# Performance work log

Measured on AMD Instinct MI355X. Metric: run time of the kernel, lower is better.

Reference implementation:

```python
import jax, jax.numpy as jnp
import numpy as np

NUM_ITER = 20
EPS = 1e-8


def _conv(x, w, pad):
    # x: [N, Cin, H, W], w: [Cout, Cin, kh, kw] (cross-correlation, like torch conv2d)
    return jax.lax.conv_general_dilated(
        x, w, window_strides=(1, 1), padding=pad,
        dimension_numbers=('NCHW', 'OIHW', 'NCHW'))


def setup_inputs() -> dict:
    key = jax.random.key(0)
    x = jax.random.normal(key, (2, 4, 3, 256, 256), dtype=jnp.float32)
    return {
        'x': x,
        'lam': jnp.array([0.02], dtype=jnp.float32),
        'tau': jnp.array([0.25], dtype=jnp.float32),
        'theta': jnp.array([0.1], dtype=jnp.float32),
        'wx': jnp.array([[-1.0, 1.0, 0.0]], dtype=jnp.float32),
        'wy': jnp.array([[-1.0], [1.0], [0.0]], dtype=jnp.float32),
    }


def reference(x, lam, tau, theta, wx, wy):
    # x: [2, B, C, H, W] -> pairs of single-channel images [NB, 2, H, W]
    F, B, C, H, W = x.shape
    NB = B * C
    xx = jnp.moveaxis(x.reshape(2, NB, H, W), 0, 1)  # [NB, 2, H, W]

    dt = x.dtype
    gx = jnp.array([[-1., 0., 1.], [-2., 0., 2.], [-1., 0., 1.]], dt) / 6.0
    gy = jnp.array([[-1., -2., -1.], [0., 0., 0.], [1., 2., 1.]], dt) / 6.0
    grad_w = jnp.stack([gx, gy])[:, None]          # [2,1,3,3] image gradient (fixed)
    gxu = jnp.array([[0., 0., 0.], [0., -1., 1.], [0., 0., 0.]], dt)
    gyu = jnp.array([[0., 0., 0.], [0., -1., 0.], [0., 1., 0.]], dt)
    grad_u_w = jnp.stack([gxu, gyu])[:, None]      # [2,1,3,3] flow gradient (fixed)
    wx_k = wx[None, None]                          # [1,1,1,3] trainable divergence stencil
    wy_k = wy[None, None]                          # [1,1,3,1]

    rho_c = (xx[:, 1] - xx[:, 0])[:, None]                       # [NB,1,H,W]
    grad_im = _conv(xx[:, 1:], grad_w, [(1, 1), (1, 1)])         # [NB,2,H,W]
    norm_grad = jnp.sum(grad_im * grad_im, axis=1, keepdims=True) + EPS

    u = jnp.zeros((NB, 2, H, W), dt)
    p1 = jnp.zeros((NB, 2, H, W), dt)
    p2 = jnp.zeros((NB, 2, H, W), dt)

    tl = theta * lam       # [1]
    tt = tau / theta       # [1]

    def div(p):  # p: [NB,2,H,W] -> [NB,1,H,W]
        return (_conv(p[:, 0:1], wx_k, [(0, 0), (1, 1)]) +
                _conv(p[:, 1:2], wy_k, [(1, 1), (0, 0)]))

    def body(carry, _):
        u, p1, p2 = carry
        rho = rho_c + jnp.sum(grad_im * u, axis=1, keepdims=True)
        th = tl * norm_grad
        v = u - jnp.where(jnp.abs(rho) < th,
                          rho * grad_im / norm_grad,
                          tl * grad_im * jnp.sign(rho))
        u0 = v[:, 0] + theta * div(p1)[:, 0]
        u1 = v[:, 1] + theta * div(p2)[:, 0]
        u = jnp.stack([u0, u1], axis=1)
        g1 = _conv(u[:, 0:1], grad_u_w, [(1, 1), (1, 1)])
        g2 = _conv(u[:, 1:2], grad_u_w, [(1, 1), (1, 1)])
        p1 = (p1 + tt * g1) / (1.0 + tt * jnp.sum(jnp.abs(g1), axis=1, keepdims=True))
        p2 = (p2 + tt * g2) / (1.0 + tt * jnp.sum(jnp.abs(g2), axis=1, keepdims=True))
        return (u, p1, p2), None

    (u, p1, p2), _ = jax.lax.scan(body, (u, p1, p2), None, length=NUM_ITER)
    return u.reshape(B, C, 2, H, W)
```

## Files before the change

### kernel.cpp

```cpp
#include <hip/hip_runtime.h>

#define W 256
#define H 256
#define HW (W*H)
#define NB 12
#define ROWS 16
#define BPI (H/ROWS)
#define NBLK (NB*BPI)
#define NTHREADS 1024
#define NUM_ITER 20
#define TVEPS 1e-8f
#define HPLANES 6
#define FLAG_MAGIC 0x5A170000


__device__ __forceinline__ float aload(const float* p) {
    return __hip_atomic_load(p, __ATOMIC_RELAXED, __HIP_MEMORY_SCOPE_AGENT);
}
__device__ __forceinline__ void astore(float* p, float v) {
    __hip_atomic_store(p, v, __ATOMIC_RELAXED, __HIP_MEMORY_SCOPE_AGENT);
}
__device__ __forceinline__ void waitflag(const int* f, int tgt) {
    while (__hip_atomic_load(f, __ATOMIC_RELAXED, __HIP_MEMORY_SCOPE_AGENT) != tgt)
        __builtin_amdgcn_s_sleep(1);
    asm volatile("" ::: "memory");
}
__device__ __forceinline__ void setflag(int* f, int tgt) {
    asm volatile("s_waitcnt vmcnt(0)" ::: "memory");
    __hip_atomic_store(f, tgt, __ATOMIC_RELAXED, __HIP_MEMORY_SCOPE_AGENT);
}
__device__ __forceinline__ float fastrcp(float x) { return __builtin_amdgcn_rcpf(x); }

#define LD4(dst, ptr) { const float4 _t = *reinterpret_cast<const float4*>(ptr); \
                        dst[0]=_t.x; dst[1]=_t.y; dst[2]=_t.z; dst[3]=_t.w; }
#define ST4(ptr, src) { float4 _t; _t.x=src[0]; _t.y=src[1]; _t.z=src[2]; _t.w=src[3]; \
                        *reinterpret_cast<float4*>(ptr) = _t; }

__global__ __launch_bounds__(NTHREADS, 1) void tvl1_uex_kernel(
    const float* __restrict__ xin,
    const float* __restrict__ lam,
    const float* __restrict__ tau,
    const float* __restrict__ theta,
    const float* __restrict__ wxv,
    const float* __restrict__ wyv,
    float* __restrict__ uout,
    float* __restrict__ halo,
    int* __restrict__ flags)
{
    __shared__ float xu0[ROWS][W];
    __shared__ float xu1[ROWS][W];
    __shared__ float xq1[ROWS][W];
    __shared__ float xq2[ROWS][W];

    const int tid  = threadIdx.x;
    const int lane = tid & 63;
    const int wv   = tid >> 6;
    const int x0   = lane << 2;
    const int b    = blockIdx.x;
    const int n    = b / BPI, bi = b % BPI;
    const int r0   = bi * ROWS;
    const int grow = r0 + wv;
    const bool notTop = (bi > 0), notBot = (bi < BPI-1);

    const float th0 = theta[0];
    const float tl  = th0 * lam[0];
    const float tt  = tau[0] / th0;
    const float wx0 = wxv[0], wx1 = wxv[1], wx2 = wxv[2];
    const float wy0 = wyv[0], wy1 = wyv[1], wy2 = wyv[2];

    const float* __restrict__ I0 = xin + (size_t)n * HW;
    const float* __restrict__ I1 = xin + (size_t)(NB + n) * HW;

    float rho[4], gxr[4], gyr[4];
    {
        #pragma unroll
        for (int c = 0; c < 4; ++c) {
            const int xc = x0 + c;
            const int idx = grow * W + xc;
            const bool xm = xc > 0, xp = xc < W-1, ym = grow > 0, yp = grow < H-1;
            float a00=0.f,a01=0.f,a02=0.f,a10=0.f,a12=0.f,a20=0.f,a21=0.f,a22=0.f;
            if (ym) { a01=I1[idx-W]; if (xm) a00=I1[idx-W-1]; if (xp) a02=I1[idx-W+1]; }
            if (xm) a10=I1[idx-1];
            if (xp) a12=I1[idx+1];
            if (yp) { a21=I1[idx+W]; if (xm) a20=I1[idx+W-1]; if (xp) a22=I1[idx+W+1]; }
            gxr[c] = ((a02-a00) + 2.f*(a12-a10) + (a22-a20)) * (1.f/6.f);
            gyr[c] = ((a20-a00) + 2.f*(a21-a01) + (a22-a02)) * (1.f/6.f);
            rho[c] = I1[idx] - I0[idx];
        }
    }

    for (int k = tid; k < ROWS*W; k += NTHREADS) {
        (&xu0[0][0])[k]=0.f; (&xu1[0][0])[k]=0.f;
        (&xq1[0][0])[k]=0.f; (&xq2[0][0])[k]=0.f;
    }
    float u0[4]={0,0,0,0}, u1[4]={0,0,0,0};
    float p1x[4]={0,0,0,0}, p1y[4]={0,0,0,0}, p2x[4]={0,0,0,0}, p2y[4]={0,0,0,0};
    __syncthreads();

    for (int it = 0; it < NUM_ITER; ++it) {
        const bool last = (it == NUM_ITER-1);

        float hym1[4]={0,0,0,0}, hym2[4]={0,0,0,0};
        float hyp1[4]={0,0,0,0}, hyp2[4]={0,0,0,0};
        if (it > 0) {
            int* fb = flags + (size_t)(it-1) * 3 * NBLK;
            const int tgt = FLAG_MAGIC | (it-1);
            if (wv == 0 && notTop) {
                if (lane == 0) waitflag(&fb[1*NBLK + (b-1)], tgt);
                const float* hu = halo + ((size_t)(it-1)*NBLK + (b-1)) * HPLANES * W;
                #pragma unroll
                for (int c = 0; c < 4; ++c) {
                    hym1[c] = aload(hu + 2*W + x0 + c);
                    hym2[c] = aload(hu + 3*W + x0 + c);
                }
            }
            if (wv == 15 && notBot) {
                if (lane == 0) waitflag(&fb[0*NBLK + (b+1)], tgt);
                const float* hd = halo + ((size_t)(it-1)*NBLK + (b+1)) * HPLANES * W;
                #pragma unroll
                for (int c = 0; c < 4; ++c) {
                    hyp1[c] = aload(hd + 0*W + x0 + c);
                    hyp2[c] = aload(hd + 1*W + x0 + c);
                }
            }
        }

        float pym1[4], pym2[4], pyp1[4], pyp2[4];
        if (wv > 0) { LD4(pym1, &xq1[wv-1][x0]); LD4(pym2, &xq2[wv-1][x0]); }
        else        { for (int c=0;c<4;++c){ pym1[c]=hym1[c]; pym2[c]=hym2[c]; } }
        if (wv < ROWS-1) { LD4(pyp1, &xq1[wv+1][x0]); LD4(pyp2, &xq2[wv+1][x0]); }
        else             { for (int c=0;c<4;++c){ pyp1[c]=hyp1[c]; pyp2[c]=hyp2[c]; } }

        float l1 = __shfl_up(p1x[3], 1);   float l2 = __shfl_up(p2x[3], 1);
        if (lane == 0) { l1 = 0.f; l2 = 0.f; }
        float r1 = __shfl_down(p1x[0], 1); float r2 = __shfl_down(p2x[0], 1);
        if (lane == 63) { r1 = 0.f; r2 = 0.f; }
        const float p1xm[4] = { l1, p1x[0], p1x[1], p1x[2] };
        const float p1xp[4] = { p1x[1], p1x[2], p1x[3], r1 };
        const float p2xm[4] = { l2, p2x[0], p2x[1], p2x[2] };
        const float p2xp[4] = { p2x[1], p2x[2], p2x[3], r2 };

        #pragma unroll
        for (int c = 0; c < 4; ++c) {
            const float r  = rho[c] + gxr[c]*u0[c] + gyr[c]*u1[c];
            const float ng = gxr[c]*gxr[c] + gyr[c]*gyr[c] + TVEPS;
            const float th = tl * ng;
            const float f  = (fabsf(r) < th) ? (r * fastrcp(ng)) : copysignf(tl, r);
            const float d1 = wx0*p1xm[c] + wx1*p1x[c] + wx2*p1xp[c]
                           + wy0*pym1[c] + wy1*p1y[c] + wy2*pyp1[c];
            const float d2 = wx0*p2xm[c] + wx1*p2x[c] + wx2*p2xp[c]
                           + wy0*pym2[c] + wy1*p2y[c] + wy2*pyp2[c];
            u0[c] = (u0[c] - f*gxr[c]) + th0*d1;
            u1[c] = (u1[c] - f*gyr[c]) + th0*d2;
        }

        if (last) {
            float* __restrict__ o0 = uout + (size_t)(2*n)   * HW + (size_t)grow * W + x0;
            float* __restrict__ o1 = uout + (size_t)(2*n+1) * HW + (size_t)grow * W + x0;
            ST4(o0, u0); ST4(o1, u1);
            break;
        }

        float* hwp = halo + ((size_t)it * NBLK + b) * HPLANES * W;
        int* fw = flags + (size_t)it * 3 * NBLK;
        const int ftgt = FLAG_MAGIC | it;
        if (wv == 0 && notTop) {
            #pragma unroll
            for (int c = 0; c < 4; ++c) {
                astore(hwp + 4*W + x0 + c, u0[c]);
                astore(hwp + 5*W + x0 + c, u1[c]);
            }
            if (lane == 0) setflag(&fw[2*NBLK + b], ftgt);
        }
        ST4(&xu0[wv][x0], u0); ST4(&xu1[wv][x0], u1);
        __syncthreads();

        float uy0[4], uy1[4];
        if (wv < ROWS-1) { LD4(uy0, &xu0[wv+1][x0]); LD4(uy1, &xu1[wv+1][x0]); }
        else if (grow == H-1) { for (int c=0;c<4;++c){ uy0[c]=0.f; uy1[c]=0.f; } }
        else {
            if (lane == 0) waitflag(&fw[2*NBLK + (b+1)], ftgt);
            const float* hd = halo + ((size_t)it*NBLK + (b+1)) * HPLANES * W;
            #pragma unroll
            for (int c = 0; c < 4; ++c) {
                uy0[c] = aload(hd + 4*W + x0 + c);
                uy1[c] = aload(hd + 5*W + x0 + c);
            }
        }
        float ur0 = __shfl_down(u0[0], 1), ur1 = __shfl_down(u1[0], 1);
        if (lane == 63) { ur0 = 0.f; ur1 = 0.f; }
        #pragma unroll
        for (int c = 0; c < 4; ++c) {
            const float uxp0 = (c < 3) ? u0[c+1] : ur0;
            const float uxp1 = (c < 3) ? u1[c+1] : ur1;
            const float g1x = uxp0 - u0[c];
            const float g1y = uy0[c] - u0[c];
            const float g2x = uxp1 - u1[c];
            const float g2y = uy1[c] - u1[c];
            const float rc1 = fastrcp(1.f + tt * (fabsf(g1x) + fabsf(g1y)));
            const float rc2 = fastrcp(1.f + tt * (fabsf(g2x) + fabsf(g2y)));
            p1x[c] = (p1x[c] + tt*g1x) * rc1;
            p1y[c] = (p1y[c] + tt*g1y) * rc1;
            p2x[c] = (p2x[c] + tt*g2x) * rc2;
            p2y[c] = (p2y[c] + tt*g2y) * rc2;
        }
        ST4(&xq1[wv][x0], p1y); ST4(&xq2[wv][x0], p2y);

        if (wv == 0 && notTop) {
            #pragma unroll
            for (int c = 0; c < 4; ++c) {
                astore(hwp + 0*W + x0 + c, p1y[c]);
                astore(hwp + 1*W + x0 + c, p2y[c]);
            }
            if (lane == 0) setflag(&fw[0*NBLK + b], ftgt);
        } else if (wv == ROWS-1 && notBot) {
            #pragma unroll
            for (int c = 0; c < 4; ++c) {
                astore(hwp + 2*W + x0 + c, p1y[c]);
                astore(hwp + 3*W + x0 + c, p2y[c]);
            }
            if (lane == 0) setflag(&fw[1*NBLK + b], ftgt);
        }
        __syncthreads();
    }
}


__global__ void precompute_kernel(const float* __restrict__ x,
                                  float* __restrict__ u,
                                  float* __restrict__ ws) {
    const int row = blockIdx.x;
    const int n = row / H, y = row % H;
    const int xx = threadIdx.x;
    const int idx = y * W + xx;
    const float* __restrict__ I0 = x + (size_t)n * HW;
    const float* __restrict__ I1 = x + (size_t)(NB + n) * HW;
    float* __restrict__ p1  = ws;
    float* __restrict__ p2  = ws + (size_t)2 * NB * HW;
    float* __restrict__ rho = ws + (size_t)4 * NB * HW;
    float* __restrict__ gxp = ws + (size_t)5 * NB * HW;
    float* __restrict__ gyp = ws + (size_t)6 * NB * HW;
    const float i1c = I1[idx];
    const bool xm = xx > 0, xp = xx < W - 1, ym = y > 0, yp = y < H - 1;
    float a00=0.f,a01=0.f,a02=0.f,a10=0.f,a12=0.f,a20=0.f,a21=0.f,a22=0.f;
    if (ym) { a01 = I1[idx-W]; if (xm) a00 = I1[idx-W-1]; if (xp) a02 = I1[idx-W+1]; }
    if (xm) a10 = I1[idx-1];
    if (xp) a12 = I1[idx+1];
    if (yp) { a21 = I1[idx+W]; if (xm) a20 = I1[idx+W-1]; if (xp) a22 = I1[idx+W+1]; }
    const float gxv = ((a02-a00) + 2.f*(a12-a10) + (a22-a20)) * (1.f/6.f);
    const float gyv = ((a20-a00) + 2.f*(a21-a01) + (a22-a02)) * (1.f/6.f);
    const size_t np = (size_t)n * HW;
    rho[np+idx] = i1c - I0[idx];
    gxp[np+idx] = gxv;
    gyp[np+idx] = gyv;
    u[(size_t)(2*n)*HW + idx] = 0.f;   u[(size_t)(2*n+1)*HW + idx] = 0.f;
    p1[(size_t)(2*n)*HW + idx] = 0.f;  p1[(size_t)(2*n+1)*HW + idx] = 0.f;
    p2[(size_t)(2*n)*HW + idx] = 0.f;  p2[(size_t)(2*n+1)*HW + idx] = 0.f;
}

__global__ void u_kernel(const float* __restrict__ ws,
                         float* __restrict__ u,
                         const float* __restrict__ lam,
                         const float* __restrict__ theta,
                         const float* __restrict__ wxv,
                         const float* __restrict__ wyv) {
    const int row = blockIdx.x;
    const int n = row / H, y = row % H;
    const int xx = threadIdx.x;
    const int idx = y * W + xx;
    const size_t np = (size_t)n * HW;
    const float* __restrict__ p1  = ws;
    const float* __restrict__ p2  = ws + (size_t)2 * NB * HW;
    const float* __restrict__ rho_c = ws + (size_t)4 * NB * HW;
    const float* __restrict__ gxp = ws + (size_t)5 * NB * HW;
    const float* __restrict__ gyp = ws + (size_t)6 * NB * HW;
    const float th0 = theta[0];
    const float tl = th0 * lam[0];
    const float wx0 = wxv[0], wx1 = wxv[1], wx2 = wxv[2];
    const float wy0 = wyv[0], wy1 = wyv[1], wy2 = wyv[2];
    const float gx = gxp[np+idx];
    const float gy = gyp[np+idx];
    float* __restrict__ u0p = u + (size_t)(2*n)*HW;
    float* __restrict__ u1p = u + (size_t)(2*n+1)*HW;
    const float u0 = u0p[idx], u1 = u1p[idx];
    const float rho = rho_c[np+idx] + gx*u0 + gy*u1;
    const float ng = gx*gx + gy*gy + TVEPS;
    const float th = tl * ng;
    float s0, s1;
    if (fabsf(rho) < th) { const float d = rho/ng; s0 = d*gx; s1 = d*gy; }
    else { const float sg = (rho > 0.f) ? 1.f : ((rho < 0.f) ? -1.f : 0.f);
           s0 = tl*gx*sg; s1 = tl*gy*sg; }
    const float v0 = u0 - s0, v1 = u1 - s1;
    const float* __restrict__ p1x = p1 + (size_t)(2*n)*HW;
    const float* __restrict__ p1y = p1 + (size_t)(2*n+1)*HW;
    const float* __restrict__ p2x = p2 + (size_t)(2*n)*HW;
    const float* __restrict__ p2y = p2 + (size_t)(2*n+1)*HW;
    float d1 = wx1*p1x[idx] + wy1*p1y[idx];
    float d2 = wx1*p2x[idx] + wy1*p2y[idx];
    if (xx > 0)     { d1 += wx0*p1x[idx-1]; d2 += wx0*p2x[idx-1]; }
    if (xx < W-1)   { d1 += wx2*p1x[idx+1]; d2 += wx2*p2x[idx+1]; }
    if (y > 0)      { d1 += wy0*p1y[idx-W]; d2 += wy0*p2y[idx-W]; }
    if (y < H-1)    { d1 += wy2*p1y[idx+W]; d2 += wy2*p2y[idx+W]; }
    u0p[idx] = v0 + th0*d1;
    u1p[idx] = v1 + th0*d2;
}

__global__ void p_kernel(const float* __restrict__ u,
                         float* __restrict__ ws,
                         const float* __restrict__ tau,
                         const float* __restrict__ theta) {
    const int row = blockIdx.x;
    const int n = row / H, y = row % H;
    const int xx = threadIdx.x;
    const int idx = y * W + xx;
    float* __restrict__ p1 = ws;
    float* __restrict__ p2 = ws + (size_t)2 * NB * HW;
    const float tt = tau[0] / theta[0];
    const float* __restrict__ u0p = u + (size_t)(2*n)*HW;
    const float* __restrict__ u1p = u + (size_t)(2*n+1)*HW;
    const float c0 = u0p[idx];
    const float g1x = ((xx < W-1) ? u0p[idx+1] : 0.f) - c0;
    const float g1y = ((y < H-1) ? u0p[idx+W] : 0.f) - c0;
    const float c1 = u1p[idx];
    const float g2x = ((xx < W-1) ? u1p[idx+1] : 0.f) - c1;
    const float g2y = ((y < H-1) ? u1p[idx+W] : 0.f) - c1;
    float* __restrict__ p1x = p1 + (size_t)(2*n)*HW;
    float* __restrict__ p1y = p1 + (size_t)(2*n+1)*HW;
    float* __restrict__ p2x = p2 + (size_t)(2*n)*HW;
    float* __restrict__ p2y = p2 + (size_t)(2*n+1)*HW;
    const float den1 = 1.f + tt * (fabsf(g1x) + fabsf(g1y));
    p1x[idx] = (p1x[idx] + tt*g1x) / den1;
    p1y[idx] = (p1y[idx] + tt*g1y) / den1;
    const float den2 = 1.f + tt * (fabsf(g2x) + fabsf(g2y));
    p2x[idx] = (p2x[idx] + tt*g2x) / den2;
    p2y[idx] = (p2y[idx] + tt*g2y) / den2;
}

extern "C" void kernel_launch(void* const* d_in, const int* in_sizes, int n_in,
                              void* d_out, int out_size, void* d_ws, size_t ws_size,
                              hipStream_t stream) {
    const float* x     = (const float*)d_in[0];
    const float* lam   = (const float*)d_in[1];
    const float* tau   = (const float*)d_in[2];
    const float* theta = (const float*)d_in[3];
    const float* wxv   = (const float*)d_in[4];
    const float* wyv   = (const float*)d_in[5];
    float* u = (float*)d_out;

    const size_t halo_floats = (size_t)(NUM_ITER-1) * NBLK * HPLANES * W;
    const size_t need = halo_floats * sizeof(float)
                      + (size_t)(NUM_ITER-1) * 3 * NBLK * sizeof(int);

    if (ws_size >= need) {
        float* halo = (float*)d_ws;
        int* flags = (int*)((char*)d_ws + halo_floats * sizeof(float));
        void* args[] = { (void*)&x, (void*)&lam, (void*)&tau, (void*)&theta,
                         (void*)&wxv, (void*)&wyv, (void*)&u, (void*)&halo, (void*)&flags };
        hipLaunchCooperativeKernel((void*)tvl1_uex_kernel, dim3(NBLK), dim3(NTHREADS),
                                   args, 0, stream);
    } else {
        float* ws = (float*)d_ws;
        const dim3 grid(NB * H);
        const dim3 block(W);
        precompute_kernel<<<grid, block, 0, stream>>>(x, u, ws);
        for (int it = 0; it < NUM_ITER; ++it) {
            u_kernel<<<grid, block, 0, stream>>>(ws, u, lam, theta, wxv, wyv);
            p_kernel<<<grid, block, 0, stream>>>(u, ws, tau, theta);
        }
    }
}
```

Measured before the change: 102.4 us.

## Temporal-block two iterations per halo exchange with redundant ghost-row compute

Restructures the persistent cooperative kernel so that neighbouring blocks exchange halos once per pair of iterations instead of every iteration. Each block recomputes up to three ghost rows redundantly (precomputing their image gradients) and exchanges a wider payload of p and u planes. The halo and flag buffers become double-buffered by superstep parity instead of one slot per iteration. This is meant to halve the inter-block flag waits and global-memory round trips, at the cost of extra redundant compute, more shared memory and more complex halo bookkeeping.

```diff
diff --git a/kernel.cpp b/kernel.cpp
--- a/kernel.cpp
+++ b/kernel.cpp
@@ -9,10 +9,18 @@
 #define NBLK (NB*BPI)
 #define NTHREADS 1024
 #define NUM_ITER 20
+#define NSUPER (NUM_ITER/2)
 #define TVEPS 1e-8f
-#define HPLANES 6
+#define NPL 28
+#define NFK 6
 #define FLAG_MAGIC 0x5A170000
 
+#define FK_U0 0
+#define FK_U1 1
+#define FK_U2 2
+#define FK_U3 3
+#define FK_D14 4
+#define FK_D15 5
 
 __device__ __forceinline__ float aload(const float* p) {
     return __hip_atomic_load(p, __ATOMIC_RELAXED, __HIP_MEMORY_SCOPE_AGENT);
@@ -35,8 +43,11 @@
                         dst[0]=_t.x; dst[1]=_t.y; dst[2]=_t.z; dst[3]=_t.w; }
 #define ST4(ptr, src) { float4 _t; _t.x=src[0]; _t.y=src[1]; _t.z=src[2]; _t.w=src[3]; \
                         *reinterpret_cast<float4*>(ptr) = _t; }
-
-__global__ __launch_bounds__(NTHREADS, 1) void tvl1_uex_kernel(
+#define LDPAY(dst, pl) { _Pragma("unroll") for (int c = 0; c < 4; ++c) dst[c] = aload(hp + (pl)*W + x0 + c); }
+#define STPAY(pl, src) { _Pragma("unroll") for (int c = 0; c < 4; ++c) astore(hw + (pl)*W + x0 + c, src[c]); }
+#define CP4(dst, src)  { _Pragma("unroll") for (int c = 0; c < 4; ++c) dst[c] = src[c]; }
+
+__global__ __launch_bounds__(NTHREADS, 1) void tvl1_ts2_kernel(
     const float* __restrict__ xin,
     const float* __restrict__ lam,
     const float* __restrict__ tau,
@@ -47,10 +58,10 @@
     float* __restrict__ halo,
     int* __restrict__ flags)
 {
-    __shared__ float xu0[ROWS][W];
-    __shared__ float xu1[ROWS][W];
-    __shared__ float xq1[ROWS][W];
-    __shared__ float xq2[ROWS][W];
+    __shared__ float xu0[ROWS+3][W];
+    __shared__ float xu1[ROWS+3][W];
+    __shared__ float xq1[ROWS+2][W];
+    __shared__ float xq2[ROWS+2][W];
 
     const int tid  = threadIdx.x;
     const int lane = tid & 63;
@@ -71,155 +82,208 @@
     const float* __restrict__ I0 = xin + (size_t)n * HW;
     const float* __restrict__ I1 = xin + (size_t)(NB + n) * HW;
 
-    float rho[4], gxr[4], gyr[4];
-    {
+    auto grad4 = [&](int row, float* rr, float* ggx, float* ggy) {
         #pragma unroll
         for (int c = 0; c < 4; ++c) {
             const int xc = x0 + c;
-            const int idx = grow * W + xc;
-            const bool xm = xc > 0, xp = xc < W-1, ym = grow > 0, yp = grow < H-1;
+            const int idx = row * W + xc;
+            const bool xm = xc > 0, xp = xc < W-1, ym = row > 0, yp = row < H-1;
             float a00=0.f,a01=0.f,a02=0.f,a10=0.f,a12=0.f,a20=0.f,a21=0.f,a22=0.f;
             if (ym) { a01=I1[idx-W]; if (xm) a00=I1[idx-W-1]; if (xp) a02=I1[idx-W+1]; }
             if (xm) a10=I1[idx-1];
             if (xp) a12=I1[idx+1];
             if (yp) { a21=I1[idx+W]; if (xm) a20=I1[idx+W-1]; if (xp) a22=I1[idx+W+1]; }
-            gxr[c] = ((a02-a00) + 2.f*(a12-a10) + (a22-a20)) * (1.f/6.f);
-            gyr[c] = ((a20-a00) + 2.f*(a21-a01) + (a22-a02)) * (1.f/6.f);
-            rho[c] = I1[idx] - I0[idx];
-        }
+            ggx[c] = ((a02-a00) + 2.f*(a12-a10) + (a22-a20)) * (1.f/6.f);
+            ggy[c] = ((a20-a00) + 2.f*(a21-a01) + (a22-a02)) * (1.f/6.f);
+            rr[c]  = I1[idx] - I0[idx];
+        }
+    };
+
+    float rho[4], gxr[4], gyr[4];
+    grad4(grow, rho, gxr, gyr);
+    float rhoH[4]={0,0,0,0}, gxH[4]={0,0,0,0}, gyH[4]={0,0,0,0};
+    {
+        const bool hg = (wv == 0 && notTop) || (wv >= 13 && notBot);
+        const int hrow = (wv == 0) ? (r0 - 1) : (r0 + ROWS + (15 - wv));
+        if (hg) grad4(hrow, rhoH, gxH, gyH);
     }
 
-    for (int k = tid; k < ROWS*W; k += NTHREADS) {
-        (&xu0[0][0])[k]=0.f; (&xu1[0][0])[k]=0.f;
-        (&xq1[0][0])[k]=0.f; (&xq2[0][0])[k]=0.f;
-    }
+    for (int k = tid; k < (ROWS+3)*W; k += NTHREADS) { (&xu0[0][0])[k]=0.f; (&xu1[0][0])[k]=0.f; }
+    for (int k = tid; k < (ROWS+2)*W; k += NTHREADS) { (&xq1[0][0])[k]=0.f; (&xq2[0][0])[k]=0.f; }
     float u0[4]={0,0,0,0}, u1[4]={0,0,0,0};
     float p1x[4]={0,0,0,0}, p1y[4]={0,0,0,0}, p2x[4]={0,0,0,0}, p2y[4]={0,0,0,0};
     __syncthreads();
 
-    for (int it = 0; it < NUM_ITER; ++it) {
-        const bool last = (it == NUM_ITER-1);
-
-        float hym1[4]={0,0,0,0}, hym2[4]={0,0,0,0};
-        float hyp1[4]={0,0,0,0}, hyp2[4]={0,0,0,0};
-        if (it > 0) {
-            int* fb = flags + (size_t)(it-1) * 3 * NBLK;
-            const int tgt = FLAG_MAGIC | (it-1);
-            if (wv == 0 && notTop) {
-                if (lane == 0) waitflag(&fb[1*NBLK + (b-1)], tgt);
-                const float* hu = halo + ((size_t)(it-1)*NBLK + (b-1)) * HPLANES * W;
-                #pragma unroll
-                for (int c = 0; c < 4; ++c) {
-                    hym1[c] = aload(hu + 2*W + x0 + c);
-                    hym2[c] = aload(hu + 3*W + x0 + c);
-                }
-            }
-            if (wv == 15 && notBot) {
-                if (lane == 0) waitflag(&fb[0*NBLK + (b+1)], tgt);
-                const float* hd = halo + ((size_t)(it-1)*NBLK + (b+1)) * HPLANES * W;
-                #pragma unroll
-                for (int c = 0; c < 4; ++c) {
-                    hyp1[c] = aload(hd + 0*W + x0 + c);
-                    hyp2[c] = aload(hd + 1*W + x0 + c);
-                }
-            }
-        }
-
-        float pym1[4], pym2[4], pyp1[4], pyp2[4];
-        if (wv > 0) { LD4(pym1, &xq1[wv-1][x0]); LD4(pym2, &xq2[wv-1][x0]); }
-        else        { for (int c=0;c<4;++c){ pym1[c]=hym1[c]; pym2[c]=hym2[c]; } }
-        if (wv < ROWS-1) { LD4(pyp1, &xq1[wv+1][x0]); LD4(pyp2, &xq2[wv+1][x0]); }
-        else             { for (int c=0;c<4;++c){ pyp1[c]=hyp1[c]; pyp2[c]=hyp2[c]; } }
-
-        float l1 = __shfl_up(p1x[3], 1);   float l2 = __shfl_up(p2x[3], 1);
+    auto ustepF = [&](const float* rr, const float* ggx, const float* ggy,
+                      float* uu0, float* uu1,
+                      const float* q1x, const float* q1ym, const float* q1yc, const float* q1yp,
+                      const float* q2x, const float* q2ym, const float* q2yc, const float* q2yp) {
+        float l1 = __shfl_up(q1x[3],1), l2 = __shfl_up(q2x[3],1);
         if (lane == 0) { l1 = 0.f; l2 = 0.f; }
-        float r1 = __shfl_down(p1x[0], 1); float r2 = __shfl_down(p2x[0], 1);
+        float r1 = __shfl_down(q1x[0],1), r2 = __shfl_down(q2x[0],1);
         if (lane == 63) { r1 = 0.f; r2 = 0.f; }
-        const float p1xm[4] = { l1, p1x[0], p1x[1], p1x[2] };
-        const float p1xp[4] = { p1x[1], p1x[2], p1x[3], r1 };
-        const float p2xm[4] = { l2, p2x[0], p2x[1], p2x[2] };
-        const float p2xp[4] = { p2x[1], p2x[2], p2x[3], r2 };
-
+        const float x1m[4]={l1,q1x[0],q1x[1],q1x[2]}, x1p[4]={q1x[1],q1x[2],q1x[3],r1};
+        const float x2m[4]={l2,q2x[0],q2x[1],q2x[2]}, x2p[4]={q2x[1],q2x[2],q2x[3],r2};
         #pragma unroll
         for (int c = 0; c < 4; ++c) {
-            const float r  = rho[c] + gxr[c]*u0[c] + gyr[c]*u1[c];
-            const float ng = gxr[c]*gxr[c] + gyr[c]*gyr[c] + TVEPS;
-            const float th = tl * ng;
-            const float f  = (fabsf(r) < th) ? (r * fastrcp(ng)) : copysignf(tl, r);
-            const float d1 = wx0*p1xm[c] + wx1*p1x[c] + wx2*p1xp[c]
-                           + wy0*pym1[c] + wy1*p1y[c] + wy2*pyp1[c];
-            const float d2 = wx0*p2xm[c] + wx1*p2x[c] + wx2*p2xp[c]
-                           + wy0*pym2[c] + wy1*p2y[c] + wy2*pyp2[c];
-            u0[c] = (u0[c] - f*gxr[c]) + th0*d1;
-            u1[c] = (u1[c] - f*gyr[c]) + th0*d2;
-        }
-
-        if (last) {
-            float* __restrict__ o0 = uout + (size_t)(2*n)   * HW + (size_t)grow * W + x0;
-            float* __restrict__ o1 = uout + (size_t)(2*n+1) * HW + (size_t)grow * W + x0;
-            ST4(o0, u0); ST4(o1, u1);
-            break;
-        }
-
-        float* hwp = halo + ((size_t)it * NBLK + b) * HPLANES * W;
-        int* fw = flags + (size_t)it * 3 * NBLK;
-        const int ftgt = FLAG_MAGIC | it;
-        if (wv == 0 && notTop) {
-            #pragma unroll
-            for (int c = 0; c < 4; ++c) {
-                astore(hwp + 4*W + x0 + c, u0[c]);
-                astore(hwp + 5*W + x0 + c, u1[c]);
-            }
-            if (lane == 0) setflag(&fw[2*NBLK + b], ftgt);
-        }
-        ST4(&xu0[wv][x0], u0); ST4(&xu1[wv][x0], u1);
-        __syncthreads();
-
-        float uy0[4], uy1[4];
-        if (wv < ROWS-1) { LD4(uy0, &xu0[wv+1][x0]); LD4(uy1, &xu1[wv+1][x0]); }
-        else if (grow == H-1) { for (int c=0;c<4;++c){ uy0[c]=0.f; uy1[c]=0.f; } }
-        else {
-            if (lane == 0) waitflag(&fw[2*NBLK + (b+1)], ftgt);
-            const float* hd = halo + ((size_t)it*NBLK + (b+1)) * HPLANES * W;
-            #pragma unroll
-            for (int c = 0; c < 4; ++c) {
-                uy0[c] = aload(hd + 4*W + x0 + c);
-                uy1[c] = aload(hd + 5*W + x0 + c);
-            }
-        }
-        float ur0 = __shfl_down(u0[0], 1), ur1 = __shfl_down(u1[0], 1);
+            const float r  = rr[c] + ggx[c]*uu0[c] + ggy[c]*uu1[c];
+            const float ng = ggx[c]*ggx[c] + ggy[c]*ggy[c] + TVEPS;
+            const float f  = (fabsf(r) < tl*ng) ? (r * fastrcp(ng)) : copysignf(tl, r);
+            const float d1 = wx0*x1m[c] + wx1*q1x[c] + wx2*x1p[c]
+                           + wy0*q1ym[c] + wy1*q1yc[c] + wy2*q1yp[c];
+            const float d2 = wx0*x2m[c] + wx1*q2x[c] + wx2*x2p[c]
+                           + wy0*q2ym[c] + wy1*q2yc[c] + wy2*q2yp[c];
+            uu0[c] = (uu0[c] - f*ggx[c]) + th0*d1;
+            uu1[c] = (uu1[c] - f*ggy[c]) + th0*d2;
+        }
+    };
+    auto pstepF = [&](const float* uc0, const float* uc1,
+                      const float* uy0, const float* uy1,
+                      float* q1x, float* q1y, float* q2x, float* q2y) {
+        float ur0 = __shfl_down(uc0[0],1), ur1 = __shfl_down(uc1[0],1);
         if (lane == 63) { ur0 = 0.f; ur1 = 0.f; }
         #pragma unroll
         for (int c = 0; c < 4; ++c) {
-            const float uxp0 = (c < 3) ? u0[c+1] : ur0;
-            const float uxp1 = (c < 3) ? u1[c+1] : ur1;
-            const float g1x = uxp0 - u0[c];
-            const float g1y = uy0[c] - u0[c];
-            const float g2x = uxp1 - u1[c];
-            const float g2y = uy1[c] - u1[c];
+            const float uxp0 = (c < 3) ? uc0[c+1] : ur0;
+            const float uxp1 = (c < 3) ? uc1[c+1] : ur1;
+            const float g1x = uxp0 - uc0[c], g1y = uy0[c] - uc0[c];
+            const float g2x = uxp1 - uc1[c], g2y = uy1[c] - uc1[c];
             const float rc1 = fastrcp(1.f + tt * (fabsf(g1x) + fabsf(g1y)));
             const float rc2 = fastrcp(1.f + tt * (fabsf(g2x) + fabsf(g2y)));
-            p1x[c] = (p1x[c] + tt*g1x) * rc1;
-            p1y[c] = (p1y[c] + tt*g1y) * rc1;
-            p2x[c] = (p2x[c] + tt*g2x) * rc2;
-            p2y[c] = (p2y[c] + tt*g2y) * rc2;
-        }
-        ST4(&xq1[wv][x0], p1y); ST4(&xq2[wv][x0], p2y);
-
+            q1x[c] = (q1x[c] + tt*g1x) * rc1;  q1y[c] = (q1y[c] + tt*g1y) * rc1;
+            q2x[c] = (q2x[c] + tt*g2x) * rc2;  q2y[c] = (q2y[c] + tt*g2y) * rc2;
+        }
+    };
+
+    for (int S = 0; S < NSUPER; ++S) {
+        const bool lastS = (S == NSUPER-1);
+        float pay[10][4];
+        #pragma unroll
+        for (int i = 0; i < 10; ++i) { pay[i][0]=0.f; pay[i][1]=0.f; pay[i][2]=0.f; pay[i][3]=0.f; }
+
+        auto ownU = [&]() {
+            float pym1[4],pym2[4],pyp1[4],pyp2[4];
+            if (wv > 0) { LD4(pym1,&xq1[wv-1][x0]); LD4(pym2,&xq2[wv-1][x0]); }
+            else        { CP4(pym1,pay[4]); CP4(pym2,pay[5]); }
+            if (wv < ROWS-1) { LD4(pyp1,&xq1[wv+1][x0]); LD4(pyp2,&xq2[wv+1][x0]); }
+            else             { CP4(pyp1,pay[2]); CP4(pyp2,pay[3]); }
+            ustepF(rho,gxr,gyr,u0,u1, p1x,pym1,p1y,pyp1, p2x,pym2,p2y,pyp2);
+            ST4(&xu0[wv][x0],u0); ST4(&xu1[wv][x0],u1);
+        };
+
+        if (wv != 0 && wv != ROWS-1) ownU();
+        if (S > 0) {
+            int* fb = flags + (size_t)((S-1)&1)*NFK*NBLK;
+            const int tgt = FLAG_MAGIC | (S-1);
+            if (wv == 0 && notTop) {
+                if (lane < 2) waitflag(&fb[(lane==0?FK_D14:FK_D15)*NBLK + (b-1)], tgt);
+                const float* hp = halo + ((size_t)((S-1)&1)*NBLK + (b-1))*((size_t)NPL*W);
+                LDPAY(pay[0],0); LDPAY(pay[1],1); LDPAY(pay[2],2); LDPAY(pay[3],3);
+                LDPAY(pay[4],4); LDPAY(pay[5],5); LDPAY(pay[6],6); LDPAY(pay[7],7);
+            } else if (wv == 15 && notBot) {
+                if (lane < 2) waitflag(&fb[(lane==0?FK_U0:FK_U1)*NBLK + (b+1)], tgt);
+                const float* hp = halo + ((size_t)((S-1)&1)*NBLK + (b+1))*((size_t)NPL*W);
+                LDPAY(pay[0],8); LDPAY(pay[1],9); LDPAY(pay[2],14); LDPAY(pay[3],15);
+                LDPAY(pay[4],16); LDPAY(pay[5],17); LDPAY(pay[6],22); LDPAY(pay[7],23);
+            } else if (wv == 14 && notBot) {
+                if (lane < 3) waitflag(&fb[(lane==0?FK_U0:(lane==1?FK_U1:FK_U2))*NBLK + (b+1)], tgt);
+                const float* hp = halo + ((size_t)((S-1)&1)*NBLK + (b+1))*((size_t)NPL*W);
+                LDPAY(pay[0],10); LDPAY(pay[1],11); LDPAY(pay[2],14); LDPAY(pay[3],15);
+                LDPAY(pay[4],16); LDPAY(pay[5],17); LDPAY(pay[6],24); LDPAY(pay[7],25);
+                LDPAY(pay[8],18); LDPAY(pay[9],19);
+            } else if (wv == 13 && notBot) {
+                if (lane < 3) waitflag(&fb[(lane==0?FK_U1:(lane==1?FK_U2:FK_U3))*NBLK + (b+1)], tgt);
+                const float* hp = halo + ((size_t)((S-1)&1)*NBLK + (b+1))*((size_t)NPL*W);
+                LDPAY(pay[0],12); LDPAY(pay[1],13); LDPAY(pay[2],16); LDPAY(pay[3],17);
+                LDPAY(pay[4],18); LDPAY(pay[5],19); LDPAY(pay[6],26); LDPAY(pay[7],27);
+                LDPAY(pay[8],20); LDPAY(pay[9],21);
+            }
+        }
+        if (wv == 0 || wv == ROWS-1) ownU();
         if (wv == 0 && notTop) {
-            #pragma unroll
-            for (int c = 0; c < 4; ++c) {
-                astore(hwp + 0*W + x0 + c, p1y[c]);
-                astore(hwp + 1*W + x0 + c, p2y[c]);
+            ustepF(rhoH,gxH,gyH, pay[6],pay[7],
+                   pay[0], pay[2],pay[4],p1y,
+                   pay[1], pay[3],pay[5],p2y);
+        } else if (wv == 15 && notBot) {
+            ustepF(rhoH,gxH,gyH, pay[6],pay[7],
+                   pay[0], p1y,pay[2],pay[4],
+                   pay[1], p2y,pay[3],pay[5]);
+            ST4(&xu0[16][x0],pay[6]); ST4(&xu1[16][x0],pay[7]);
+        } else if ((wv == 14 || wv == 13) && notBot) {
+            ustepF(rhoH,gxH,gyH, pay[6],pay[7],
+                   pay[0], pay[2],pay[4],pay[8],
+                   pay[1], pay[3],pay[5],pay[9]);
+            const int hr = (wv == 14) ? 17 : 18;
+            ST4(&xu0[hr][x0],pay[6]); ST4(&xu1[hr][x0],pay[7]);
+        }
+        __syncthreads();
+
+        {
+            float uy0[4],uy1[4];
+            LD4(uy0,&xu0[wv+1][x0]); LD4(uy1,&xu1[wv+1][x0]);
+            pstepF(u0,u1, uy0,uy1, p1x,p1y,p2x,p2y);
+            ST4(&xq1[wv][x0],p1y); ST4(&xq2[wv][x0],p2y);
+        }
+        if (wv == 0 && notTop) {
+            pstepF(pay[6],pay[7], u0,u1, pay[0],pay[4], pay[1],pay[5]);
+        } else if (wv == 15 && notBot) {
+            float uy0[4],uy1[4]; LD4(uy0,&xu0[17][x0]); LD4(uy1,&xu1[17][x0]);
+            pstepF(pay[6],pay[7], uy0,uy1, pay[0],pay[2], pay[1],pay[3]);
+            ST4(&xq1[16][x0],pay[2]); ST4(&xq2[16][x0],pay[3]);
+        } else if (wv == 14 && notBot) {
+            float uy0[4],uy1[4]; LD4(uy0,&xu0[18][x0]); LD4(uy1,&xu1[18][x0]);
+            pstepF(pay[6],pay[7], uy0,uy1, pay[0],pay[4], pay[1],pay[5]);
+            ST4(&xq1[17][x0],pay[4]); ST4(&xq2[17][x0],pay[5]);
+        }
+        __syncthreads();
+
+        {
+            float pym1[4],pym2[4],pyp1[4],pyp2[4];
+            if (wv > 0) { LD4(pym1,&xq1[wv-1][x0]); LD4(pym2,&xq2[wv-1][x0]); }
+            else        { CP4(pym1,pay[4]); CP4(pym2,pay[5]); }
+            LD4(pyp1,&xq1[wv+1][x0]); LD4(pyp2,&xq2[wv+1][x0]);
+            ustepF(rho,gxr,gyr,u0,u1, p1x,pym1,p1y,pyp1, p2x,pym2,p2y,pyp2);
+        }
+        if (lastS) {
+            float* __restrict__ o0 = uout + (size_t)(2*n)   * HW + (size_t)grow * W + x0;
+            float* __restrict__ o1 = uout + (size_t)(2*n+1) * HW + (size_t)grow * W + x0;
+            ST4(o0,u0); ST4(o1,u1);
+            break;
+        }
+        ST4(&xu0[wv][x0],u0); ST4(&xu1[wv][x0],u1);
+        if (wv == 15 && notBot) {
+            float yp1[4],yp2[4]; LD4(yp1,&xq1[17][x0]); LD4(yp2,&xq2[17][x0]);
+            ustepF(rhoH,gxH,gyH, pay[6],pay[7],
+                   pay[0], p1y,pay[2],yp1,
+                   pay[1], p2y,pay[3],yp2);
+            ST4(&xu0[16][x0],pay[6]); ST4(&xu1[16][x0],pay[7]);
+        }
+        __syncthreads();
+
+        {
+            float uy0[4],uy1[4];
+            LD4(uy0,&xu0[wv+1][x0]); LD4(uy1,&xu1[wv+1][x0]);
+            pstepF(u0,u1, uy0,uy1, p1x,p1y,p2x,p2y);
+            ST4(&xq1[wv][x0],p1y); ST4(&xq2[wv][x0],p2y);
+        }
+        {
+            float* hw = halo + ((size_t)(S&1)*NBLK + b)*((size_t)NPL*W);
+            int* fw = flags + (size_t)(S&1)*NFK*NBLK;
+            const int ft = FLAG_MAGIC | S;
+            if (notTop) {
+                if (wv == 0)      { STPAY(8,p1x);  STPAY(9,p2x);  STPAY(14,p1y); STPAY(15,p2y);
+                                    STPAY(22,u0);  STPAY(23,u1);  if (lane==0) setflag(&fw[FK_U0*NBLK+b],ft); }
+                else if (wv == 1) { STPAY(10,p1x); STPAY(11,p2x); STPAY(16,p1y); STPAY(17,p2y);
+                                    STPAY(24,u0);  STPAY(25,u1);  if (lane==0) setflag(&fw[FK_U1*NBLK+b],ft); }
+                else if (wv == 2) { STPAY(12,p1x); STPAY(13,p2x); STPAY(18,p1y); STPAY(19,p2y);
+                                    STPAY(26,u0);  STPAY(27,u1);  if (lane==0) setflag(&fw[FK_U2*NBLK+b],ft); }
+                else if (wv == 3) { STPAY(20,p1y); STPAY(21,p2y); if (lane==0) setflag(&fw[FK_U3*NBLK+b],ft); }
             }
-            if (lane == 0) setflag(&fw[0*NBLK + b], ftgt);
-        } else if (wv == ROWS-1 && notBot) {
-            #pragma unroll
-            for (int c = 0; c < 4; ++c) {
-                astore(hwp + 2*W + x0 + c, p1y[c]);
-                astore(hwp + 3*W + x0 + c, p2y[c]);
+            if (notBot) {
+                if (wv == 14)      { STPAY(2,p1y); STPAY(3,p2y); if (lane==0) setflag(&fw[FK_D14*NBLK+b],ft); }
+                else if (wv == 15) { STPAY(0,p1x); STPAY(1,p2x); STPAY(4,p1y); STPAY(5,p2y);
+                                     STPAY(6,u0);  STPAY(7,u1);  if (lane==0) setflag(&fw[FK_D15*NBLK+b],ft); }
             }
-            if (lane == 0) setflag(&fw[1*NBLK + b], ftgt);
         }
         __syncthreads();
     }
@@ -291,16 +355,16 @@
     else { const float sg = (rho > 0.f) ? 1.f : ((rho < 0.f) ? -1.f : 0.f);
            s0 = tl*gx*sg; s1 = tl*gy*sg; }
     const float v0 = u0 - s0, v1 = u1 - s1;
-    const float* __restrict__ p1x = p1 + (size_t)(2*n)*HW;
-    const float* __restrict__ p1y = p1 + (size_t)(2*n+1)*HW;
-    const float* __restrict__ p2x = p2 + (size_t)(2*n)*HW;
-    const float* __restrict__ p2y = p2 + (size_t)(2*n+1)*HW;
-    float d1 = wx1*p1x[idx] + wy1*p1y[idx];
-    float d2 = wx1*p2x[idx] + wy1*p2y[idx];
-    if (xx > 0)     { d1 += wx0*p1x[idx-1]; d2 += wx0*p2x[idx-1]; }
-    if (xx < W-1)   { d1 += wx2*p1x[idx+1]; d2 += wx2*p2x[idx+1]; }
-    if (y > 0)      { d1 += wy0*p1y[idx-W]; d2 += wy0*p2y[idx-W]; }
-    if (y < H-1)    { d1 += wy2*p1y[idx+W]; d2 += wy2*p2y[idx+W]; }
+    const float* __restrict__ p1xp = p1 + (size_t)(2*n)*HW;
+    const float* __restrict__ p1yp = p1 + (size_t)(2*n+1)*HW;
+    const float* __restrict__ p2xp = p2 + (size_t)(2*n)*HW;
+    const float* __restrict__ p2yp = p2 + (size_t)(2*n+1)*HW;
+    float d1 = wx1*p1xp[idx] + wy1*p1yp[idx];
+    float d2 = wx1*p2xp[idx] + wy1*p2yp[idx];
+    if (xx > 0)     { d1 += wx0*p1xp[idx-1]; d2 += wx0*p2xp[idx-1]; }
+    if (xx < W-1)   { d1 += wx2*p1xp[idx+1]; d2 += wx2*p2xp[idx+1]; }
+    if (y > 0)      { d1 += wy0*p1yp[idx-W]; d2 += wy0*p2yp[idx-W]; }
+    if (y < H-1)    { d1 += wy2*p1yp[idx+W]; d2 += wy2*p2yp[idx+W]; }
     u0p[idx] = v0 + th0*d1;
     u1p[idx] = v1 + th0*d2;
 }
@@ -324,16 +388,16 @@
     const float c1 = u1p[idx];
     const float g2x = ((xx < W-1) ? u1p[idx+1] : 0.f) - c1;
     const float g2y = ((y < H-1) ? u1p[idx+W] : 0.f) - c1;
-    float* __restrict__ p1x = p1 + (size_t)(2*n)*HW;
-    float* __restrict__ p1y = p1 + (size_t)(2*n+1)*HW;
-    float* __restrict__ p2x = p2 + (size_t)(2*n)*HW;
-    float* __restrict__ p2y = p2 + (size_t)(2*n+1)*HW;
+    float* __restrict__ p1xp = p1 + (size_t)(2*n)*HW;
+    float* __restrict__ p1yp = p1 + (size_t)(2*n+1)*HW;
+    float* __restrict__ p2xp = p2 + (size_t)(2*n)*HW;
+    float* __restrict__ p2yp = p2 + (size_t)(2*n+1)*HW;
     const float den1 = 1.f + tt * (fabsf(g1x) + fabsf(g1y));
-    p1x[idx] = (p1x[idx] + tt*g1x) / den1;
-    p1y[idx] = (p1y[idx] + tt*g1y) / den1;
+    p1xp[idx] = (p1xp[idx] + tt*g1x) / den1;
+    p1yp[idx] = (p1yp[idx] + tt*g1y) / den1;
     const float den2 = 1.f + tt * (fabsf(g2x) + fabsf(g2y));
-    p2x[idx] = (p2x[idx] + tt*g2x) / den2;
-    p2y[idx] = (p2y[idx] + tt*g2y) / den2;
+    p2xp[idx] = (p2xp[idx] + tt*g2x) / den2;
+    p2yp[idx] = (p2yp[idx] + tt*g2y) / den2;
 }
 
 extern "C" void kernel_launch(void* const* d_in, const int* in_sizes, int n_in,
@@ -347,16 +411,15 @@
     const float* wyv   = (const float*)d_in[5];
     float* u = (float*)d_out;
 
-    const size_t halo_floats = (size_t)(NUM_ITER-1) * NBLK * HPLANES * W;
-    const size_t need = halo_floats * sizeof(float)
-                      + (size_t)(NUM_ITER-1) * 3 * NBLK * sizeof(int);
+    const size_t halo_floats = (size_t)2 * NBLK * NPL * W;
+    const size_t need = halo_floats * sizeof(float) + (size_t)2 * NFK * NBLK * sizeof(int);
 
     if (ws_size >= need) {
         float* halo = (float*)d_ws;
         int* flags = (int*)((char*)d_ws + halo_floats * sizeof(float));
         void* args[] = { (void*)&x, (void*)&lam, (void*)&tau, (void*)&theta,
                          (void*)&wxv, (void*)&wyv, (void*)&u, (void*)&halo, (void*)&flags };
-        hipLaunchCooperativeKernel((void*)tvl1_uex_kernel, dim3(NBLK), dim3(NTHREADS),
+        hipLaunchCooperativeKernel((void*)tvl1_ts2_kernel, dim3(NBLK), dim3(NTHREADS),
                                    args, 0, stream);
     } else {
         float* ws = (float*)d_ws;
```

Measured after the change: 178.6 us. 1.74x slower.
